# Kernel optimization log

Hardware: AMD Instinct MI355X
Metric: run time of the kernel (lower is better)

## Reference

```python
import jax, jax.numpy as jnp
import numpy as np
from jax import lax

SD = 16  # sample_duration
POOL_KS = (SD, SD * 3 // 4, SD // 2, SD // 4)  # (16, 12, 8, 4)


def conv3d_same(x, w, b):
    # x: [B,C,T,H,W], w: [O,I,3,3,3]
    y = lax.conv_general_dilated(
        x, w, window_strides=(1, 1, 1), padding=[(1, 1), (1, 1), (1, 1)],
        dimension_numbers=("NCDHW", "OIDHW", "NCDHW"))
    return y + b[None, :, None, None, None]


def maxpool_t(x, k):
    # MaxPool3d((k,1,1), stride=1): max over sliding temporal window
    return lax.reduce_window(x, -jnp.inf, lax.max,
                             (1, 1, k, 1, 1), (1, 1, 1, 1, 1), "VALID")


def head1x1(x, w, b):
    # 1x1x1 Conv3d as einsum; x: [B,C,T,H,W], w: [O,C]
    return jnp.einsum("bcthw,oc->bothw", x, w) + b[None, :, None, None, None]


def cls_prob(score):
    # _RPN.reshape(x,2) -> softmax(dim=1) -> reshape back to [B,30,T,H,W]
    B, C, T, H, W = score.shape
    s2 = score.reshape(B, 2, (C * T) // 2, H, W)
    p = jax.nn.softmax(s2, axis=1)
    return p.reshape(B, C, T, H, W)


def setup_inputs() -> dict:
    key = jax.random.key(0)
    ks = jax.random.split(key, 12)
    din, B, H, W = 512, 2, 28, 28
    s = 0.05
    return {
        "base_feat": jax.random.normal(ks[0], (B, din, SD, H, W), jnp.float32),
        "im_info": jnp.ones((B, 3), jnp.float32) * 448.0,
        "gt_boxes": jax.random.uniform(ks[1], (B, 20, 5), jnp.float32),
        "gt_rois": jax.random.uniform(ks[2], (B, 20, SD, 5), jnp.float32),
        "W_conv": jax.random.normal(ks[3], (din, din, 3, 3, 3), jnp.float32) * 0.01,
        "b_conv": jnp.zeros((din,), jnp.float32),
        "W_cls": jax.random.normal(ks[4], (30, din), jnp.float32) * s,
        "b_cls": jnp.zeros((30,), jnp.float32),
        "W_bbox": jax.random.normal(ks[5], (960, din), jnp.float32) * s,
        "b_bbox": jnp.zeros((960,), jnp.float32),
        "W_bbox_34": jax.random.normal(ks[6], (720, din), jnp.float32) * s,
        "b_bbox_34": jnp.zeros((720,), jnp.float32),
        "W_bbox_2": jax.random.normal(ks[7], (480, din), jnp.float32) * s,
        "b_bbox_2": jnp.zeros((480,), jnp.float32),
        "W_bbox_4": jax.random.normal(ks[8], (240, din), jnp.float32) * s,
        "b_bbox_4": jnp.zeros((240,), jnp.float32),
    }


def reference(base_feat, im_info, gt_boxes, gt_rois,
              W_conv, b_conv, W_cls, b_cls,
              W_bbox, b_bbox, W_bbox_34, b_bbox_34,
              W_bbox_2, b_bbox_2, W_bbox_4, b_bbox_4):
    # RPN conv + relu
    x = jax.nn.relu(conv3d_same(base_feat, W_conv, b_conv))
    # four temporal max-pool branches (T' = 1, 5, 9, 13)
    pools = [maxpool_t(x, k) for k in POOL_KS]
    # NOTE: original code applies the SAME RPN_cls_score conv to all branches
    probs = tuple(cls_prob(head1x1(p, W_cls, b_cls)) for p in pools)
    bbox_ws = [(W_bbox, b_bbox), (W_bbox_34, b_bbox_34),
               (W_bbox_2, b_bbox_2), (W_bbox_4, b_bbox_4)]
    bboxes = tuple(head1x1(p, w, b) for p, (w, b) in zip(pools, bbox_ws))
    return probs + bboxes
```

## Files before the change

kernel.cpp:

```cpp
#include <hip/hip_runtime.h>

typedef unsigned short u16;
typedef unsigned int   u32;
typedef __bf16  bf16x8 __attribute__((ext_vector_type(8)));
typedef float   f32x4  __attribute__((ext_vector_type(4)));

__device__ __forceinline__ float bf2f(u16 u) {
    u32 v = ((u32)u) << 16;
    return __builtin_bit_cast(float, v);
}
__device__ __forceinline__ u16 f2bf(float f) {
    u32 u = __builtin_bit_cast(u32, f);
    return (u16)((u + 0x7FFFu + ((u >> 16) & 1u)) >> 16);
}
__device__ __forceinline__ float ldf(const void* p, long i, int f32) {
    return f32 ? ((const float*)p)[i] : bf2f(((const u16*)p)[i]);
}
__device__ __forceinline__ int is_f32(const u32* im) {
    return im[0] == 0x43E00000u;
}
__device__ __forceinline__ void gl2lds16(const u16* g, u16* l) {
    __builtin_amdgcn_global_load_lds(
        (const __attribute__((address_space(1))) void*)g,
        (__attribute__((address_space(3))) void*)l, 16, 0, 0);
}

__global__ void pad_zero_fill(const void* __restrict__ src, u16* __restrict__ xpad,
                              const u32* __restrict__ im)
{
    __shared__ u16 lds[56 * 40];
    if (blockIdx.x >= 7168) {
        int i = (blockIdx.x - 7168) * 256 + threadIdx.x;
        if (i < 230400) {
            int c8 = i & 63; int pos = i >> 6;
            int p = pos % 900; pos /= 900;
            int t = (pos & 1) * 17; int b = pos >> 1;
            long o = (((long)(b * 18 + t) * 900) + p) * 512 + c8 * 8;
            *(uint4*)&xpad[o] = uint4{0u, 0u, 0u, 0u};
            return;
        }
        i -= 230400;
        if (i < 122880) {
            int c8 = i & 63; int pos = i >> 6;
            int w = pos % 30; pos /= 30;
            int h = (pos & 1) * 29; pos >>= 1;
            int t = pos % 16 + 1; int b = pos / 16;
            long o = ((((long)(b * 18 + t) * 30 + h) * 30) + w) * 512 + c8 * 8;
            *(uint4*)&xpad[o] = uint4{0u, 0u, 0u, 0u};
            return;
        }
        i -= 122880;
        if (i < 114688) {
            int c8 = i & 63; int pos = i >> 6;
            int w = (pos & 1) * 29; pos >>= 1;
            int h = pos % 28 + 1; pos /= 28;
            int t = pos % 16 + 1; int b = pos / 16;
            long o = ((((long)(b * 18 + t) * 30 + h) * 30) + w) * 512 + c8 * 8;
            *(uint4*)&xpad[o] = uint4{0u, 0u, 0u, 0u};
        }
        return;
    }
    const int f32 = is_f32(im);
    int blk = blockIdx.x;
    const int h2  = blk % 14;  blk /= 14;
    const int c32 = blk & 15;  blk >>= 4;
    const int t   = blk & 15;
    const int b   = blk >> 4;
    const int tid = threadIdx.x;
    const long sbase = ((long)(b * 512 + c32 * 32) * 16 + t) * 784 + h2 * 56;
    #pragma unroll
    for (int it = tid; it < 1792; it += 256) {
        const int c = it / 56, p = it - c * 56;
        float v = f32 ? ((const float*)src)[sbase + (long)c * 12544 + p]
                      : bf2f(((const u16*)src)[sbase + (long)c * 12544 + p]);
        lds[p * 40 + c] = f2bf(v);
    }
    __syncthreads();
    if (tid < 224) {
        const int p = tid >> 2, g = tid & 3;
        const int h = h2 * 2 + p / 28, w = p % 28;
        const long o = (((long)(b * 18 + t + 1) * 30 + h + 1) * 30 + (w + 1)) * 512
                       + c32 * 32 + g * 8;
        *(uint4*)&xpad[o] = *(const uint4*)&lds[p * 40 + g * 8];
    }
}

__global__ void wt_transform(const void* __restrict__ wconv, u16* __restrict__ wt,
                             const u32* __restrict__ im)
{
    const int f32 = is_f32(im);
    __shared__ u16 lds[256 * 28];
    const int tid = threadIdx.x;
    const int pair_base = blockIdx.x * 256;
    const long s0 = (long)pair_base * 27;
    for (int it = tid; it < 256 * 27; it += 256) {
        const int p = it / 27, o = it - p * 27;
        float v = f32 ? ((const float*)wconv)[s0 + it]
                      : bf2f(((const u16*)wconv)[s0 + it]);
        lds[p * 28 + o] = f2bf(v);
    }
    __syncthreads();
    #pragma unroll
    for (int off = 0; off < 27; ++off)
        wt[(long)off * 262144 + pair_base + tid] = lds[tid * 28 + off];
}

__global__ void cvt_all(const void* s0, const void* s1, const void* s2,
                        const void* s3, const void* s4,
                        const void* b0, const void* b1, const void* b2,
                        const void* b3, const void* b4, const void* b5,
                        u16* __restrict__ whd, float* __restrict__ bfs,
                        const u32* __restrict__ im)
{
    const int f32 = is_f32(im);
    int i = blockIdx.x * 256 + threadIdx.x;
    if (i < 1244160) {
        const void* s; long j;
        if      (i < 15360)   { s = s0; j = i; }
        else if (i < 506880)  { s = s1; j = i - 15360; }
        else if (i < 875520)  { s = s2; j = i - 506880; }
        else if (i < 1121280) { s = s3; j = i - 875520; }
        else                  { s = s4; j = i - 1121280; }
        whd[i] = f2bf(ldf(s, j, f32));
        return;
    }
    i -= 1244160;
    if (i >= 2942) return;
    float v;
    if      (i < 512)  v = ldf(b0, i, f32);
    else if (i < 542)  v = ldf(b1, i - 512, f32);
    else if (i < 1502) v = ldf(b2, i - 542, f32);
    else if (i < 2222) v = ldf(b3, i - 1502, f32);
    else if (i < 2702) v = ldf(b4, i - 2222, f32);
    else               v = ldf(b5, i - 2702, f32);
    bfs[i] = v;
}

__global__ __launch_bounds__(512, 2) void conv_gemm256(
    const u16* __restrict__ xpad, const u16* __restrict__ wt,
    const float* __restrict__ bfs, u16* __restrict__ y)
{
    __shared__ u16 smem[65536];
    const int tid = threadIdx.x;

    const int bx  = blockIdx.x;
    const int xcd = bx & 7, pos = bx >> 3;
    const int L   = (xcd < 4 ? xcd * 25 : 100 + (xcd - 4) * 24) + pos;
    const int m_base = (L & 1) * 256;
    const int n_base = (L >> 1) * 256;

    const int rq8 = tid >> 3;
    const int sw  = (((tid & 7) ^ (rq8 & 7))) * 8;
    const u16* pa = wt + (long)(m_base + rq8) * 512 + sw;

    long sbj[4];
    #pragma unroll
    for (int j = 0; j < 4; ++j) {
        const int n = n_base + j * 64 + rq8;
        int b = n / 12544, r = n % 12544;
        int t = r / 784,   q = r % 784;
        int h = q / 28,    w = q % 28;
        const int sa = ((b * 18 + t) * 30 + h) * 30 + w;
        sbj[j] = (long)sa * 512 + sw;
    }

    const int lane = tid & 63, wid = tid >> 6;
    const int l16 = lane & 15, quad = lane >> 4;
    const int wm = wid >> 2;
    const int wn = wid & 3;
    const int x7 = l16 & 7;
    const int o0 = (quad ^ x7) * 8;
    const int o1 = ((4 + quad) ^ x7) * 8;
    int rowA[8], rowB[4];
    #pragma unroll
    for (int mi = 0; mi < 8; ++mi) rowA[mi] = (wm * 128 + mi * 16 + l16) * 64;
    #pragma unroll
    for (int ni = 0; ni < 4; ++ni) rowB[ni] = 16384 + (wn * 64 + ni * 16 + l16) * 64;

    f32x4 acc[8][4] = {};

    {
        u16* dst = smem;
        #pragma unroll
        for (int j = 0; j < 4; ++j)
            gl2lds16(pa + (long)j * 32768, dst + j * 4096 + tid * 8);
        #pragma unroll
        for (int j = 0; j < 4; ++j)
            gl2lds16(xpad + sbj[j], dst + 16384 + j * 4096 + tid * 8);
    }

    for (int kt = 0; kt < 216; ++kt) {
        asm volatile("s_waitcnt vmcnt(0)" ::: "memory");
        asm volatile("s_barrier" ::: "memory");
        const u16* buf = smem + (kt & 1) * 32768;

        bf16x8 af[8], bfr[4];
        #pragma unroll
        for (int mi = 0; mi < 4; ++mi)
            af[mi] = *(const bf16x8*)&buf[rowA[mi] + o0];
        #pragma unroll
        for (int ni = 0; ni < 4; ++ni)
            bfr[ni] = *(const bf16x8*)&buf[rowB[ni] + o0];
        #pragma unroll
        for (int mi = 4; mi < 8; ++mi)
            af[mi] = *(const bf16x8*)&buf[rowA[mi] + o0];

        if (kt < 215) {
            const int kts = kt + 1;
            const int tap = kts >> 3, kc = kts & 7;
            const int kd = tap / 9, r9 = tap - kd * 9;
            const int kh = r9 / 3,  kw = r9 - kh * 3;
            const long aoff = (long)tap * 262144 + kc * 64;
            const long boff = (long)(kd * 900 + kh * 30 + kw) * 512 + kc * 64;
            u16* dst = smem + ((kts & 1) << 15);
            #pragma unroll
            for (int j = 0; j < 4; ++j)
                gl2lds16(pa + aoff + (long)j * 32768, dst + j * 4096 + tid * 8);
            #pragma unroll
            for (int j = 0; j < 4; ++j)
                gl2lds16(xpad + sbj[j] + boff, dst + 16384 + j * 4096 + tid * 8);
        }

        __builtin_amdgcn_s_setprio(1);
        #pragma unroll
        for (int mi = 0; mi < 8; ++mi)
            #pragma unroll
            for (int ni = 0; ni < 4; ++ni)
                acc[mi][ni] = __builtin_amdgcn_mfma_f32_16x16x32_bf16(
                    af[mi], bfr[ni], acc[mi][ni], 0, 0, 0);
        __builtin_amdgcn_s_setprio(0);

        bf16x8 ag[8], bgr[4];
        #pragma unroll
        for (int mi = 0; mi < 8; ++mi)
            ag[mi] = *(const bf16x8*)&buf[rowA[mi] + o1];
        #pragma unroll
        for (int ni = 0; ni < 4; ++ni)
            bgr[ni] = *(const bf16x8*)&buf[rowB[ni] + o1];

        __builtin_amdgcn_s_setprio(1);
        #pragma unroll
        for (int mi = 0; mi < 8; ++mi)
            #pragma unroll
            for (int ni = 0; ni < 4; ++ni)
                acc[mi][ni] = __builtin_amdgcn_mfma_f32_16x16x32_bf16(
                    ag[mi], bgr[ni], acc[mi][ni], 0, 0, 0);
        __builtin_amdgcn_s_setprio(0);
    }

    #pragma unroll
    for (int mi = 0; mi < 8; ++mi) {
        const int mrow = m_base + wm * 128 + mi * 16 + quad * 4;
        float bias[4];
        #pragma unroll
        for (int r = 0; r < 4; ++r) bias[r] = bfs[mrow + r];
        #pragma unroll
        for (int ni = 0; ni < 4; ++ni) {
            const int ng = n_base + wn * 64 + ni * 16 + l16;
            f32x4 a = acc[mi][ni];
            u16 o0v = f2bf(fmaxf(a[0] + bias[0], 0.f));
            u16 o1v = f2bf(fmaxf(a[1] + bias[1], 0.f));
            u16 o2v = f2bf(fmaxf(a[2] + bias[2], 0.f));
            u16 o3v = f2bf(fmaxf(a[3] + bias[3], 0.f));
            uint2 pv;
            pv.x = (u32)o0v | ((u32)o1v << 16);
            pv.y = (u32)o2v | ((u32)o3v << 16);
            *(uint2*)&y[(long)ng * 512 + mrow] = pv;
        }
    }
}

__device__ __forceinline__ uint2 max4(uint2 A, uint2 Bv)
{
    const u16* a = (const u16*)&A;
    const u16* b = (const u16*)&Bv;
    uint2 R;
    u16* r = (u16*)&R;
    #pragma unroll
    for (int i = 0; i < 4; ++i) r[i] = (bf2f(a[i]) >= bf2f(b[i])) ? a[i] : b[i];
    return R;
}

__global__ void pool_all(const u16* __restrict__ y, u16* __restrict__ p4,
                         u16* __restrict__ p8, u16* __restrict__ p12,
                         u16* __restrict__ p16)
{
    int g = blockIdx.x * 256 + threadIdx.x;
    if (g >= 200704) return;
    const int c4 = g & 127;
    int pos = g >> 7;
    const int hw = pos % 784; const int b = pos / 784;
    const u16* src = y + ((long)(b * 16) * 784 + hw) * 512 + c4 * 4;
    uint2 v[16];
    #pragma unroll
    for (int t = 0; t < 16; ++t)
        v[t] = *(const uint2*)(src + (long)t * 401408);
    uint2 pr[15];
    #pragma unroll
    for (int t = 0; t < 15; ++t) pr[t] = max4(v[t], v[t + 1]);
    uint2 qd[13];
    #pragma unroll
    for (int t = 0; t < 13; ++t) qd[t] = max4(pr[t], pr[t + 2]);
    uint2 e8[9];
    #pragma unroll
    for (int t = 0; t < 9; ++t) e8[t] = max4(qd[t], qd[t + 4]);
    uint2 e12[5];
    #pragma unroll
    for (int t = 0; t < 5; ++t) e12[t] = max4(e8[t], qd[t + 8]);
    uint2 e16 = max4(e8[0], e8[8]);

    const long col = (long)hw * 512 + c4 * 4;
    #pragma unroll
    for (int t = 0; t < 13; ++t)
        *(uint2*)&p4[((long)(b * 13 + t) * 784) * 512 + col] = qd[t];
    #pragma unroll
    for (int t = 0; t < 9; ++t)
        *(uint2*)&p8[((long)(b * 9 + t) * 784) * 512 + col] = e8[t];
    #pragma unroll
    for (int t = 0; t < 5; ++t)
        *(uint2*)&p12[((long)(b * 5 + t) * 784) * 512 + col] = e12[t];
    *(uint2*)&p16[((long)b * 784) * 512 + col] = e16;
}

__global__ __launch_bounds__(256, 2) void heads_gemm(
    const u16* __restrict__ p16, const u16* __restrict__ p12,
    const u16* __restrict__ p8,  const u16* __restrict__ p4,
    const u16* __restrict__ wcls, const u16* __restrict__ wb1,
    const u16* __restrict__ wb34, const u16* __restrict__ wb2,
    const u16* __restrict__ wb4,  const float* __restrict__ bfs,
    void* __restrict__ outv, const u32* __restrict__ im)
{
    const int f32 = is_f32(im);
    int bid = blockIdx.x;
    const u16* pool; const u16* wbp; int Ti, CH, nt, mt; long boff, coff, ooff;
    if (bid < 104)      {             nt = bid % 13;  mt = bid / 13;  pool = p16; wbp = wb1;  Ti = 1;  CH = 960; boff = 542;  coff = 0;      ooff = 1317120; }
    else if (bid < 476) { bid -= 104; nt = bid % 62;  mt = bid / 62;  pool = p12; wbp = wb34; Ti = 5;  CH = 720; boff = 1502; coff = 47040;  ooff = 2822400; }
    else if (bid < 920) { bid -= 476; nt = bid % 111; mt = bid / 111; pool = p8;  wbp = wb2;  Ti = 9;  CH = 480; boff = 2222; coff = 282240; ooff = 8467200; }
    else                { bid -= 920; nt = bid % 160; mt = bid / 160; pool = p4;  wbp = wb4;  Ti = 13; CH = 240; boff = 2702; coff = 705600; ooff = 15240960; }
    const int M = 30 + CH;
    const int THW = Ti * 784;
    const int N = 2 * THW;
    const int n_base = nt * 128;
    const int m_base = mt * 128;

    __shared__ u16 lds[24576];
    const int tid = threadIdx.x;
    const int lane = tid & 63;
    const int wid  = tid >> 6;
    const int quad = lane >> 4;
    const int l16  = lane & 15;
    const int wm = (wid & 1) * 64;
    const int wn = (wid >> 1) * 64;

    const int srow = tid >> 2;
    const int kk   = (((tid & 3) ^ ((tid >> 3) & 3))) * 8;

    const u16* arow[2]; const u16* brow[2];
    #pragma unroll
    for (int i = 0; i < 2; ++i) {
        int m = m_base + i * 64 + srow; if (m > M - 1) m = M - 1;
        arow[i] = ((m < 30) ? (wcls + m * 512) : (wbp + (m - 30) * 512)) + kk;
        int n = n_base + i * 64 + srow; if (n > N - 1) n = N - 1;
        brow[i] = pool + (long)n * 512 + kk;
    }

    const int co = (quad ^ ((l16 >> 1) & 3)) * 8;
    int rowA[4], rowB[4];
    #pragma unroll
    for (int i = 0; i < 4; ++i) {
        rowA[i] = (wm + i * 16 + l16) * 32 + co;
        rowB[i] = 4096 + (wn + i * 16 + l16) * 32 + co;
    }

    #pragma unroll
    for (int i = 0; i < 2; ++i)
        gl2lds16(arow[i], &lds[i * 2048 + tid * 8]);
    #pragma unroll
    for (int i = 0; i < 2; ++i)
        gl2lds16(brow[i], &lds[4096 + i * 2048 + tid * 8]);
    #pragma unroll
    for (int i = 0; i < 2; ++i)
        gl2lds16(arow[i] + 32, &lds[8192 + i * 2048 + tid * 8]);
    #pragma unroll
    for (int i = 0; i < 2; ++i)
        gl2lds16(brow[i] + 32, &lds[8192 + 4096 + i * 2048 + tid * 8]);

    f32x4 acc[4][4] = {};
    int cb = 0;
    for (int kc = 0; kc < 15; ++kc) {
        asm volatile("s_waitcnt vmcnt(4)" ::: "memory");
        asm volatile("s_barrier" ::: "memory");
        const u16* buf = lds + cb * 8192;
        bf16x8 af[4], bfr[4];
        #pragma unroll
        for (int mi = 0; mi < 4; ++mi)
            af[mi]  = *(const bf16x8*)&buf[rowA[mi]];
        #pragma unroll
        for (int ni = 0; ni < 4; ++ni)
            bfr[ni] = *(const bf16x8*)&buf[rowB[ni]];
        if (kc < 14) {
            const int kcol = (kc + 2) * 32;
            int nb = cb + 2; if (nb >= 3) nb -= 3;
            u16* dst = lds + nb * 8192 + tid * 8;
            #pragma unroll
            for (int i = 0; i < 2; ++i)
                gl2lds16(arow[i] + kcol, dst + i * 2048);
            #pragma unroll
            for (int i = 0; i < 2; ++i)
                gl2lds16(brow[i] + kcol, dst + 4096 + i * 2048);
        }
        __builtin_amdgcn_s_setprio(1);
        #pragma unroll
        for (int mi = 0; mi < 4; ++mi)
            #pragma unroll
            for (int ni = 0; ni < 4; ++ni)
                acc[mi][ni] = __builtin_amdgcn_mfma_f32_16x16x32_bf16(
                    af[mi], bfr[ni], acc[mi][ni], 0, 0, 0);
        __builtin_amdgcn_s_setprio(0);
        cb = (cb + 1 == 3) ? 0 : cb + 1;
    }
    {
        asm volatile("s_waitcnt vmcnt(0)" ::: "memory");
        asm volatile("s_barrier" ::: "memory");
        const u16* buf = lds + cb * 8192;
        bf16x8 af[4], bfr[4];
        #pragma unroll
        for (int mi = 0; mi < 4; ++mi)
            af[mi]  = *(const bf16x8*)&buf[rowA[mi]];
        #pragma unroll
        for (int ni = 0; ni < 4; ++ni)
            bfr[ni] = *(const bf16x8*)&buf[rowB[ni]];
        #pragma unroll
        for (int mi = 0; mi < 4; ++mi)
            #pragma unroll
            for (int ni = 0; ni < 4; ++ni)
                acc[mi][ni] = __builtin_amdgcn_mfma_f32_16x16x32_bf16(
                    af[mi], bfr[ni], acc[mi][ni], 0, 0, 0);
    }

    __syncthreads();
    float* smf = (float*)lds;
    const float* bcls = bfs + 512;
    const float* bb   = bfs + boff;
    #pragma unroll
    for (int mi = 0; mi < 4; ++mi) {
        const int mrow = m_base + wm + mi * 16 + quad * 4;
        #pragma unroll
        for (int ni = 0; ni < 4; ++ni) {
            const int ng = n_base + wn + ni * 16 + l16;
            if (ng >= N) continue;
            const int b  = ng / THW;
            const int rr = ng % THW;
            f32x4 a = acc[mi][ni];
            #pragma unroll
            for (int r = 0; r < 4; ++r) {
                const int m = mrow + r;
                if (m >= M) break;
                if (m < 30) {
                    smf[m * 128 + (wn + ni * 16 + l16)] = a[r] + bcls[m];
                } else {
                    const float v = a[r] + bb[m - 30];
                    const long oi = ooff + ((long)(b * CH + (m - 30))) * THW + rr;
                    if (f32) ((float*)outv)[oi] = v;
                    else     ((u16*)outv)[oi]   = f2bf(v);
                }
            }
        }
    }
    __syncthreads();
    if (m_base == 0) {
        for (int p = tid; p < 1920; p += 256) {
            const int j = p >> 7, col = p & 127;
            const int ng = n_base + col;
            if (ng >= N) continue;
            const float s0 = smf[j * 128 + col];
            const float s1 = smf[(j + 15) * 128 + col];
            const float mx = fmaxf(s0, s1);
            const float e0 = __expf(s0 - mx), e1 = __expf(s1 - mx);
            const float inv = 1.0f / (e0 + e1);
            const int b = ng / THW, rr = ng % THW;
            const long i0 = coff + ((long)(b * 30 + j)) * THW + rr;
            const long i1 = coff + ((long)(b * 30 + j + 15)) * THW + rr;
            if (f32) {
                ((float*)outv)[i0] = e0 * inv;
                ((float*)outv)[i1] = e1 * inv;
            } else {
                ((u16*)outv)[i0] = f2bf(e0 * inv);
                ((u16*)outv)[i1] = f2bf(e1 * inv);
            }
        }
    }
}

extern "C" void kernel_launch(void* const* d_in, const int* in_sizes, int n_in,
                              void* d_out, int out_size, void* d_ws, size_t ws_size,
                              hipStream_t stream)
{
    const void* base_feat = d_in[0];
    const u32*  im_info   = (const u32*)d_in[1];
    const void* W_conv    = d_in[4];
    const void* b_conv    = d_in[5];
    const void* W_cls     = d_in[6];
    const void* b_cls     = d_in[7];
    const void* W_bbox    = d_in[8];
    const void* b_bbox    = d_in[9];
    const void* W_bbox34  = d_in[10];
    const void* b_bbox34  = d_in[11];
    const void* W_bbox2   = d_in[12];
    const void* b_bbox2   = d_in[13];
    const void* W_bbox4   = d_in[14];
    const void* b_bbox4   = d_in[15];

    char* ws = (char*)d_ws;
    u16*   xpad = (u16*)  (ws + 0);
    u16*   wt   = (u16*)  (ws + 33177600);
    u16*   y    = (u16*)  (ws + 47333376);
    u16*   p4   = (u16*)  (ws + 73023488);
    u16*   p8   = (u16*)  (ws + 93896704);
    u16*   p12  = (u16*)  (ws + 108347392);
    u16*   p16  = (u16*)  (ws + 116375552);
    u16*   whd  = (u16*)  (ws + 123249728);
    float* bfs  = (float*)(ws + 125738048);

    u16* w_cls_b  = whd;
    u16* w_b1_b   = whd + 15360;
    u16* w_b34_b  = whd + 506880;
    u16* w_b2_b   = whd + 875520;
    u16* w_b4_b   = whd + 1121280;

    pad_zero_fill<<<8996, 256, 0, stream>>>(base_feat, xpad, im_info);
    wt_transform<<<1024, 256, 0, stream>>>(W_conv, wt, im_info);
    cvt_all<<<4873, 256, 0, stream>>>(W_cls, W_bbox, W_bbox34, W_bbox2, W_bbox4,
                                      b_conv, b_cls, b_bbox, b_bbox34, b_bbox2,
                                      b_bbox4, whd, bfs, im_info);

    conv_gemm256<<<196, 512, 0, stream>>>(xpad, wt, bfs, y);

    pool_all<<<784, 256, 0, stream>>>(y, p4, p8, p12, p16);

    heads_gemm<<<1400, 256, 0, stream>>>(p16, p12, p8, p4,
                                         w_cls_b, w_b1_b, w_b34_b, w_b2_b, w_b4_b,
                                         bfs, d_out, im_info);
}
```

Before: 562.3 us.

## Retile conv GEMM to 256x224 tiles with 224 blocks and merge weight-prep kernels

The conv implicit GEMM tile changes from 256x256 to 256x224. The grid grows from 196 to 224 blocks, which covers the 256 CUs more fully, and warps are rearranged into a 4x2 layout with 4x7 MFMA fragments. B-tile staging is restricted to 448 threads, and the last N indices are clamped, since 25088 splits evenly into 112 column tiles of 224. The weight transform and the head-weight conversion kernels are merged into one launch to save a kernel launch. The cost is a lower MFMA-to-LDS-read ratio per warp (4+7 fragment loads for 28 MFMAs versus 8+4 for 32) and a slightly smaller data reuse per block.

After: 541.9 us. -3.6%, faster.

```diff
diff --git a/kernel.cpp b/kernel.cpp
--- a/kernel.cpp
+++ b/kernel.cpp
@@ -85,35 +85,33 @@
     }
 }
 
-__global__ void wt_transform(const void* __restrict__ wconv, u16* __restrict__ wt,
-                             const u32* __restrict__ im)
+__global__ void wt_cvt_all(const void* __restrict__ wconv, u16* __restrict__ wt,
+                           const void* s0, const void* s1, const void* s2,
+                           const void* s3, const void* s4,
+                           const void* b0, const void* b1, const void* b2,
+                           const void* b3, const void* b4, const void* b5,
+                           u16* __restrict__ whd, float* __restrict__ bfs,
+                           const u32* __restrict__ im)
 {
     const int f32 = is_f32(im);
     __shared__ u16 lds[256 * 28];
     const int tid = threadIdx.x;
-    const int pair_base = blockIdx.x * 256;
-    const long s0 = (long)pair_base * 27;
-    for (int it = tid; it < 256 * 27; it += 256) {
-        const int p = it / 27, o = it - p * 27;
-        float v = f32 ? ((const float*)wconv)[s0 + it]
-                      : bf2f(((const u16*)wconv)[s0 + it]);
-        lds[p * 28 + o] = f2bf(v);
-    }
-    __syncthreads();
-    #pragma unroll
-    for (int off = 0; off < 27; ++off)
-        wt[(long)off * 262144 + pair_base + tid] = lds[tid * 28 + off];
-}
-
-__global__ void cvt_all(const void* s0, const void* s1, const void* s2,
-                        const void* s3, const void* s4,
-                        const void* b0, const void* b1, const void* b2,
-                        const void* b3, const void* b4, const void* b5,
-                        u16* __restrict__ whd, float* __restrict__ bfs,
-                        const u32* __restrict__ im)
-{
-    const int f32 = is_f32(im);
-    int i = blockIdx.x * 256 + threadIdx.x;
+    if (blockIdx.x < 1024) {
+        const int pair_base = blockIdx.x * 256;
+        const long s0l = (long)pair_base * 27;
+        for (int it = tid; it < 256 * 27; it += 256) {
+            const int p = it / 27, o = it - p * 27;
+            float v = f32 ? ((const float*)wconv)[s0l + it]
+                          : bf2f(((const u16*)wconv)[s0l + it]);
+            lds[p * 28 + o] = f2bf(v);
+        }
+        __syncthreads();
+        #pragma unroll
+        for (int off = 0; off < 27; ++off)
+            wt[(long)off * 262144 + pair_base + tid] = lds[tid * 28 + off];
+        return;
+    }
+    int i = (blockIdx.x - 1024) * 256 + tid;
     if (i < 1244160) {
         const void* s; long j;
         if      (i < 15360)   { s = s0; j = i; }
@@ -140,14 +138,13 @@
     const u16* __restrict__ xpad, const u16* __restrict__ wt,
     const float* __restrict__ bfs, u16* __restrict__ y)
 {
-    __shared__ u16 smem[65536];
+    __shared__ u16 smem[61440];
     const int tid = threadIdx.x;
 
     const int bx  = blockIdx.x;
-    const int xcd = bx & 7, pos = bx >> 3;
-    const int L   = (xcd < 4 ? xcd * 25 : 100 + (xcd - 4) * 24) + pos;
+    const int L   = (bx & 7) * 28 + (bx >> 3);
     const int m_base = (L & 1) * 256;
-    const int n_base = (L >> 1) * 256;
+    const int n_base = (L >> 1) * 224;
 
     const int rq8 = tid >> 3;
     const int sw  = (((tid & 7) ^ (rq8 & 7))) * 8;
@@ -156,54 +153,55 @@
     long sbj[4];
     #pragma unroll
     for (int j = 0; j < 4; ++j) {
-        const int n = n_base + j * 64 + rq8;
+        int n = n_base + j * 56 + rq8;
+        if (n > 25087) n = 25087;
         int b = n / 12544, r = n % 12544;
         int t = r / 784,   q = r % 784;
         int h = q / 28,    w = q % 28;
         const int sa = ((b * 18 + t) * 30 + h) * 30 + w;
         sbj[j] = (long)sa * 512 + sw;
     }
+    const bool stgB = (tid < 448);
 
     const int lane = tid & 63, wid = tid >> 6;
     const int l16 = lane & 15, quad = lane >> 4;
-    const int wm = wid >> 2;
-    const int wn = wid & 3;
+    const int wm = wid >> 1;
+    const int wn = wid & 1;
     const int x7 = l16 & 7;
     const int o0 = (quad ^ x7) * 8;
     const int o1 = ((4 + quad) ^ x7) * 8;
-    int rowA[8], rowB[4];
-    #pragma unroll
-    for (int mi = 0; mi < 8; ++mi) rowA[mi] = (wm * 128 + mi * 16 + l16) * 64;
-    #pragma unroll
-    for (int ni = 0; ni < 4; ++ni) rowB[ni] = 16384 + (wn * 64 + ni * 16 + l16) * 64;
-
-    f32x4 acc[8][4] = {};
+    int rowA[4], rowB[7];
+    #pragma unroll
+    for (int mi = 0; mi < 4; ++mi) rowA[mi] = (wm * 64 + mi * 16 + l16) * 64;
+    #pragma unroll
+    for (int ni = 0; ni < 7; ++ni) rowB[ni] = 16384 + (wn * 112 + ni * 16 + l16) * 64;
+
+    f32x4 acc[4][7] = {};
 
     {
         u16* dst = smem;
         #pragma unroll
         for (int j = 0; j < 4; ++j)
             gl2lds16(pa + (long)j * 32768, dst + j * 4096 + tid * 8);
-        #pragma unroll
-        for (int j = 0; j < 4; ++j)
-            gl2lds16(xpad + sbj[j], dst + 16384 + j * 4096 + tid * 8);
+        if (stgB) {
+            #pragma unroll
+            for (int j = 0; j < 4; ++j)
+                gl2lds16(xpad + sbj[j], dst + 16384 + j * 3584 + tid * 8);
+        }
     }
 
     for (int kt = 0; kt < 216; ++kt) {
         asm volatile("s_waitcnt vmcnt(0)" ::: "memory");
         asm volatile("s_barrier" ::: "memory");
-        const u16* buf = smem + (kt & 1) * 32768;
-
-        bf16x8 af[8], bfr[4];
+        const u16* buf = smem + (kt & 1) * 30720;
+
+        bf16x8 af[4], bfr[7];
         #pragma unroll
         for (int mi = 0; mi < 4; ++mi)
             af[mi] = *(const bf16x8*)&buf[rowA[mi] + o0];
         #pragma unroll
-        for (int ni = 0; ni < 4; ++ni)
+        for (int ni = 0; ni < 7; ++ni)
             bfr[ni] = *(const bf16x8*)&buf[rowB[ni] + o0];
-        #pragma unroll
-        for (int mi = 4; mi < 8; ++mi)
-            af[mi] = *(const bf16x8*)&buf[rowA[mi] + o0];
 
         if (kt < 215) {
             const int kts = kt + 1;
@@ -212,51 +210,53 @@
             const int kh = r9 / 3,  kw = r9 - kh * 3;
             const long aoff = (long)tap * 262144 + kc * 64;
             const long boff = (long)(kd * 900 + kh * 30 + kw) * 512 + kc * 64;
-            u16* dst = smem + ((kts & 1) << 15);
+            u16* dst = smem + (kts & 1) * 30720;
             #pragma unroll
             for (int j = 0; j < 4; ++j)
                 gl2lds16(pa + aoff + (long)j * 32768, dst + j * 4096 + tid * 8);
-            #pragma unroll
-            for (int j = 0; j < 4; ++j)
-                gl2lds16(xpad + sbj[j] + boff, dst + 16384 + j * 4096 + tid * 8);
+            if (stgB) {
+                #pragma unroll
+                for (int j = 0; j < 4; ++j)
+                    gl2lds16(xpad + sbj[j] + boff, dst + 16384 + j * 3584 + tid * 8);
+            }
         }
 
         __builtin_amdgcn_s_setprio(1);
         #pragma unroll
-        for (int mi = 0; mi < 8; ++mi)
-            #pragma unroll
-            for (int ni = 0; ni < 4; ++ni)
+        for (int mi = 0; mi < 4; ++mi)
+            #pragma unroll
+            for (int ni = 0; ni < 7; ++ni)
                 acc[mi][ni] = __builtin_amdgcn_mfma_f32_16x16x32_bf16(
                     af[mi], bfr[ni], acc[mi][ni], 0, 0, 0);
         __builtin_amdgcn_s_setprio(0);
 
-        bf16x8 ag[8], bgr[4];
-        #pragma unroll
-        for (int mi = 0; mi < 8; ++mi)
+        bf16x8 ag[4], bgr[7];
+        #pragma unroll
+        for (int mi = 0; mi < 4; ++mi)
             ag[mi] = *(const bf16x8*)&buf[rowA[mi] + o1];
         #pragma unroll
-        for (int ni = 0; ni < 4; ++ni)
+        for (int ni = 0; ni < 7; ++ni)
             bgr[ni] = *(const bf16x8*)&buf[rowB[ni] + o1];
 
         __builtin_amdgcn_s_setprio(1);
         #pragma unroll
-        for (int mi = 0; mi < 8; ++mi)
-            #pragma unroll
-            for (int ni = 0; ni < 4; ++ni)
+        for (int mi = 0; mi < 4; ++mi)
+            #pragma unroll
+            for (int ni = 0; ni < 7; ++ni)
                 acc[mi][ni] = __builtin_amdgcn_mfma_f32_16x16x32_bf16(
                     ag[mi], bgr[ni], acc[mi][ni], 0, 0, 0);
         __builtin_amdgcn_s_setprio(0);
     }
 
     #pragma unroll
-    for (int mi = 0; mi < 8; ++mi) {
-        const int mrow = m_base + wm * 128 + mi * 16 + quad * 4;
+    for (int mi = 0; mi < 4; ++mi) {
+        const int mrow = m_base + wm * 64 + mi * 16 + quad * 4;
         float bias[4];
         #pragma unroll
         for (int r = 0; r < 4; ++r) bias[r] = bfs[mrow + r];
         #pragma unroll
-        for (int ni = 0; ni < 4; ++ni) {
-            const int ng = n_base + wn * 64 + ni * 16 + l16;
+        for (int ni = 0; ni < 7; ++ni) {
+            const int ng = n_base + wn * 112 + ni * 16 + l16;
             f32x4 a = acc[mi][ni];
             u16 o0v = f2bf(fmaxf(a[0] + bias[0], 0.f));
             u16 o1v = f2bf(fmaxf(a[1] + bias[1], 0.f));
@@ -529,12 +529,12 @@
     u16* w_b4_b   = whd + 1121280;
 
     pad_zero_fill<<<8996, 256, 0, stream>>>(base_feat, xpad, im_info);
-    wt_transform<<<1024, 256, 0, stream>>>(W_conv, wt, im_info);
-    cvt_all<<<4873, 256, 0, stream>>>(W_cls, W_bbox, W_bbox34, W_bbox2, W_bbox4,
-                                      b_conv, b_cls, b_bbox, b_bbox34, b_bbox2,
-                                      b_bbox4, whd, bfs, im_info);
-
-    conv_gemm256<<<196, 512, 0, stream>>>(xpad, wt, bfs, y);
+    wt_cvt_all<<<5897, 256, 0, stream>>>(W_conv, wt,
+                                         W_cls, W_bbox, W_bbox34, W_bbox2, W_bbox4,
+                                         b_conv, b_cls, b_bbox, b_bbox34, b_bbox2,
+                                         b_bbox4, whd, bfs, im_info);
+
+    conv_gemm256<<<224, 512, 0, stream>>>(xpad, wt, bfs, y);
 
     pool_all<<<784, 256, 0, stream>>>(y, p4, p8, p12, p16);
 
```
